# Performance work log

Measured on AMD Instinct MI355X. Metric: run time of the kernel, lower is better.

Reference implementation:

```python
import jax, jax.numpy as jnp
import numpy as np

B, S, E, H = 4, 2048, 1024, 16
D = E // H  # head dim = 64


def setup_inputs() -> dict:
    key = jax.random.key(0)
    ks = jax.random.split(key, 8)
    scale = 0.02
    return {
        "query": jax.random.normal(ks[0], (B, S, E), jnp.float32),
        "keys": jax.random.normal(ks[1], (B, S, E), jnp.float32),
        "values": jax.random.normal(ks[2], (B, S, E), jnp.float32),
        "mask": jnp.ones((B, 1, 1, S), jnp.int32),
        "Wq": jax.random.normal(ks[3], (D, D), jnp.float32) * scale,
        "Wk": jax.random.normal(ks[4], (D, D), jnp.float32) * scale,
        "Wv": jax.random.normal(ks[5], (D, D), jnp.float32) * scale,
        "Wf": jax.random.normal(ks[6], (E, E), jnp.float32) * scale,
        "bf": jax.random.normal(ks[7], (E,), jnp.float32) * scale,
    }


def reference(query, keys, values, mask, Wq, Wk, Wv, Wf, bf):
    b, sq, _ = query.shape
    sk = keys.shape[1]
    # reshape to heads: [b, s, H, D]
    q = query.reshape(b, sq, H, D)
    k = keys.reshape(b, sk, H, D)
    v = values.reshape(b, sk, H, D)
    # per-head linear projections (torch Linear: x @ W.T, no bias)
    q = jnp.einsum('bshd,ed->bshe', q, Wq)
    k = jnp.einsum('bshd,ed->bshe', k, Wk)
    v = jnp.einsum('bshd,ed->bshe', v, Wv)
    # scores [b, h, q, k]
    scores = jnp.einsum('bqhd,bkhd->bhqk', q, k)
    scores = jnp.where(mask == 0, -jnp.inf, scores)
    attn = jax.nn.softmax(scores / jnp.sqrt(jnp.float32(D)), axis=3)
    # context [b, q, h, d] -> [b, q, E]
    ctx = jnp.einsum('bhqk,bkhd->bqhd', attn, v).reshape(b, sq, E)
    return ctx @ Wf.T + bf
```

## Files before the change

kernel.cpp:

```cpp
#include <hip/hip_runtime.h>

#define B_ 4
#define S_ 2048
#define E_ 1024
#define H_ 16
#define D_ 64

typedef unsigned short u16;
typedef unsigned int u32;
typedef __bf16 bf16x8 __attribute__((ext_vector_type(8)));
typedef float f32x4 __attribute__((ext_vector_type(4)));
typedef u16 u16x8 __attribute__((ext_vector_type(8)));
typedef u16 u16x4 __attribute__((ext_vector_type(4)));

#if defined(__has_builtin)
#if __has_builtin(__builtin_amdgcn_exp2f)
#define EXP2F(x) __builtin_amdgcn_exp2f(x)
#else
#define EXP2F(x) exp2f(x)
#endif
#else
#define EXP2F(x) exp2f(x)
#endif

__device__ __forceinline__ u16 bfbits(float f) {
  __bf16 h = (__bf16)f;
  return __builtin_bit_cast(u16, h);
}
__device__ __forceinline__ f32x4 mfma16(bf16x8 a, bf16x8 b, f32x4 c) {
  return __builtin_amdgcn_mfma_f32_16x16x32_bf16(a, b, c, 0, 0, 0);
}
__device__ __forceinline__ bf16x8 lds_ld8(const u16* base, int off) {
  return *reinterpret_cast<const bf16x8*>(reinterpret_cast<const char*>(base) + off);
}
__device__ __forceinline__ void gload_lds16(const u16* g, u16* l) {
  __builtin_amdgcn_global_load_lds((const __attribute__((address_space(1))) void*)g,
                                   (__attribute__((address_space(3))) void*)l, 16, 0, 0);
}

__global__ __launch_bounds__(256) void proj_kernel(
    const float* __restrict__ qin, const float* __restrict__ kin, const float* __restrict__ vin,
    const float* __restrict__ Wq, const float* __restrict__ Wk, const float* __restrict__ Wv,
    const float* __restrict__ Wf,
    u16* __restrict__ qo, u16* __restrict__ ko, u16* __restrict__ vo, u16* __restrict__ wfo)
{
  const int t = threadIdx.x;
  const int tensor = blockIdx.z >> 2, b = blockIdx.z & 3;

  if (tensor == 3) {
    int chunk = ((blockIdx.z & 3) * 16 + blockIdx.y) * 16 + blockIdx.x;
    int i = chunk * 256 + t;
    float4 f = reinterpret_cast<const float4*>(Wf)[i];
    u16x4 h4;
    h4[0] = bfbits(f.x); h4[1] = bfbits(f.y); h4[2] = bfbits(f.z); h4[3] = bfbits(f.w);
    reinterpret_cast<u16x4*>(wfo)[i] = h4;
    return;
  }

  __shared__ __align__(16) u16 Al[128 * 64];
  __shared__ __align__(16) u16 Wl[64 * 64];
  const int w = t >> 6, l = t & 63, lg = l >> 4, ln = l & 15;
  const int h = blockIdx.y, s0 = blockIdx.x * 128;

  const float* x; const float* W; float scale;
  if (tensor == 0)      { x = qin; W = Wq; scale = 0.125f * 1.44269504f; }
  else if (tensor == 1) { x = kin; W = Wk; scale = 1.0f; }
  else                  { x = vin; W = Wv; scale = 1.0f; }

  {
    const int e = t >> 2, d0 = (t & 3) * 16;
    const float4* wr = reinterpret_cast<const float4*>(W + e * 64 + d0);
    float4 f0 = wr[0], f1 = wr[1], f2 = wr[2], f3 = wr[3];
    u16x8 p0, p1;
    p0[0]=bfbits(f0.x*scale); p0[1]=bfbits(f0.y*scale); p0[2]=bfbits(f0.z*scale); p0[3]=bfbits(f0.w*scale);
    p0[4]=bfbits(f1.x*scale); p0[5]=bfbits(f1.y*scale); p0[6]=bfbits(f1.z*scale); p0[7]=bfbits(f1.w*scale);
    p1[0]=bfbits(f2.x*scale); p1[1]=bfbits(f2.y*scale); p1[2]=bfbits(f2.z*scale); p1[3]=bfbits(f2.w*scale);
    p1[4]=bfbits(f3.x*scale); p1[5]=bfbits(f3.y*scale); p1[6]=bfbits(f3.z*scale); p1[7]=bfbits(f3.w*scale);
    *reinterpret_cast<u16x8*>(reinterpret_cast<char*>(Wl) + ((e*128 + d0*2     ) ^ ((e & 7) << 4))) = p0;
    *reinterpret_cast<u16x8*>(reinterpret_cast<char*>(Wl) + ((e*128 + d0*2 + 16) ^ ((e & 7) << 4))) = p1;
  }
  {
    const int row = t >> 1, d0 = (t & 1) * 32;
    const float4* xr = reinterpret_cast<const float4*>(x + ((size_t)(b * S_ + s0 + row)) * E_ + h * D_ + d0);
    #pragma unroll
    for (int c = 0; c < 4; ++c) {
      float4 f0 = xr[2 * c], f1 = xr[2 * c + 1];
      u16x8 pk;
      pk[0]=bfbits(f0.x); pk[1]=bfbits(f0.y); pk[2]=bfbits(f0.z); pk[3]=bfbits(f0.w);
      pk[4]=bfbits(f1.x); pk[5]=bfbits(f1.y); pk[6]=bfbits(f1.z); pk[7]=bfbits(f1.w);
      *reinterpret_cast<u16x8*>(reinterpret_cast<char*>(Al) +
          ((row * 128 + (d0 + 8 * c) * 2) ^ ((row & 7) << 4))) = pk;
    }
  }
  __syncthreads();

  bf16x8 wb[4][2];
  #pragma unroll
  for (int nn = 0; nn < 4; ++nn) {
    int brow = nn * 16 + ln;
    int bo = (brow * 128 + lg * 16) ^ ((ln & 7) << 4);
    wb[nn][0] = lds_ld8(Wl, bo);
    wb[nn][1] = lds_ld8(Wl, bo ^ 64);
  }
  f32x4 acc[2][4] = {};
  #pragma unroll
  for (int sub = 0; sub < 2; ++sub) {
    int arow = 32 * w + 16 * sub + ln;
    int ao = (arow * 128 + lg * 16) ^ ((ln & 7) << 4);
    bf16x8 a0 = lds_ld8(Al, ao), a1 = lds_ld8(Al, ao ^ 64);
    #pragma unroll
    for (int nn = 0; nn < 4; ++nn) {
      acc[sub][nn] = mfma16(a0, wb[nn][0], acc[sub][nn]);
      acc[sub][nn] = mfma16(a1, wb[nn][1], acc[sub][nn]);
    }
  }

  if (tensor < 2) {
    u16* o = (tensor == 0) ? qo : ko;
    const size_t hb = ((size_t)(b * H_ + h)) * (S_ * D_);
    #pragma unroll
    for (int sub = 0; sub < 2; ++sub)
      #pragma unroll
      for (int nn = 0; nn < 4; ++nn)
        #pragma unroll
        for (int r = 0; r < 4; ++r)
          o[hb + (size_t)(s0 + 32*w + 16*sub + 4*lg + r) * D_ + nn*16 + ln] = bfbits(acc[sub][nn][r]);
  } else {
    const size_t hb = ((size_t)(b * H_ + h)) * (D_ * S_);
    #pragma unroll
    for (int sub = 0; sub < 2; ++sub)
      #pragma unroll
      for (int nn = 0; nn < 4; ++nn)
        #pragma unroll
        for (int r = 0; r < 4; ++r) {
          int scol = s0 + 32*w + 16*sub + 4*lg + r;
          int sl = scol & 63;
          int c = (sl & 3) | (((sl >> 4) & 1) << 2) | (((sl >> 2) & 3) << 3) | ((sl >> 5) << 5);
          vo[hb + (size_t)(nn*16 + ln) * S_ + (scol & ~63) + c] = bfbits(acc[sub][nn][r]);
        }
  }
}

#define COMPUTE_TILE(KT, BUF)                                                  \
  {                                                                            \
    const u16* Kc = &Kl[BUF][0];                                               \
    const u16* Vc = &Vl[BUF][0];                                               \
    f32x4 sc[2][4];                                                            \
    __builtin_amdgcn_s_setprio(1);                                             \
    _Pragma("unroll")                                                          \
    for (int kn = 0; kn < 4; ++kn) {                                           \
      int o0 = ((ln * 128 + lg * 16) ^ ((ln & 7) << 4)) + kn * 2048;           \
      bf16x8 ka0 = lds_ld8(Kc, o0), ka1 = lds_ld8(Kc, o0 ^ 64);                \
      _Pragma("unroll")                                                        \
      for (int sub = 0; sub < 2; ++sub) {                                      \
        f32x4 z = {0.f, 0.f, 0.f, 0.f};                                        \
        z = mfma16(ka0, qb[sub][0], z);                                        \
        z = mfma16(ka1, qb[sub][1], z);                                        \
        sc[sub][kn] = z;                                                       \
      }                                                                        \
    }                                                                          \
    __builtin_amdgcn_s_setprio(0);                                             \
    if (!allone) {                                                             \
      const int kv0 = (KT) * 64;                                               \
      _Pragma("unroll")                                                        \
      for (int kn = 0; kn < 4; ++kn) {                                         \
        const int4 m4 = *reinterpret_cast<const int4*>(                        \
            mask + b * S_ + kv0 + kn * 16 + lg * 4);                           \
        const int* mp = reinterpret_cast<const int*>(&m4);                     \
        _Pragma("unroll")                                                      \
        for (int r = 0; r < 4; ++r)                                            \
          if (mp[r] == 0) { sc[0][kn][r] = -1e30f; sc[1][kn][r] = -1e30f; }    \
      }                                                                        \
    }                                                                          \
    bf16x8 pa[2][2];                                                           \
    _Pragma("unroll")                                                          \
    for (int sub = 0; sub < 2; ++sub)                                          \
      _Pragma("unroll")                                                        \
      for (int kn = 0; kn < 4; ++kn)                                           \
        _Pragma("unroll")                                                      \
        for (int r = 0; r < 4; ++r)                                            \
          pa[sub][kn >> 1][(kn & 1) * 4 + r] = (__bf16)EXP2F(sc[sub][kn][r]);  \
    __builtin_amdgcn_s_setprio(1);                                             \
    _Pragma("unroll")                                                          \
    for (int sub = 0; sub < 2; ++sub) {                                        \
      lacc[sub] = mfma16(pa[sub][0], ones, lacc[sub]);                         \
      lacc[sub] = mfma16(pa[sub][1], ones, lacc[sub]);                         \
    }                                                                          \
    _Pragma("unroll")                                                          \
    for (int kh = 0; kh < 2; ++kh)                                             \
      _Pragma("unroll")                                                        \
      for (int dn = 0; dn < 4; ++dn) {                                         \
        int vo0 = ((ln * 128 + 16 * lg + 64 * kh) ^ ((ln & 7) << 4)) + dn * 2048; \
        bf16x8 vb = lds_ld8(Vc, vo0);                                          \
        _Pragma("unroll")                                                      \
        for (int sub = 0; sub < 2; ++sub)                                      \
          oacc[sub][dn] = mfma16(pa[sub][kh], vb, oacc[sub][dn]);              \
      }                                                                        \
    __builtin_amdgcn_s_setprio(0);                                             \
  }

__global__ __launch_bounds__(512, 4) void attn_kernel(
    const u16* __restrict__ qw,
    const u16* __restrict__ kw,
    const u16* __restrict__ vtw,
    const int* __restrict__ mask,
    u16* __restrict__ ctx)
{
  __shared__ __align__(16) u16 Kl[4][64 * 64];
  __shared__ __align__(16) u16 Vl[4][64 * 64];
  __shared__ int s_allone;

  const int t = threadIdx.x, w = t >> 6, l = t & 63, lg = l >> 4, ln = l & 15;
  const int hb = blockIdx.x;
  const int b = hb >> 4;
  const int q0 = blockIdx.y * 256;
  const size_t koff = (size_t)hb * (S_ * D_);
  const size_t voff = (size_t)hb * (D_ * S_);

  if (t == 0) s_allone = 1;
  __syncthreads();

  const int srow = t >> 3, scol = (t & 7) ^ ((t >> 3) & 7);
  const u16* kg = kw + koff + srow * D_ + scol * 8;
  const u16* vg = vtw + voff + (size_t)srow * S_ + scol * 8;
  u16* kd0 = &Kl[0][0] + t * 8;
  u16* vd0 = &Vl[0][0] + t * 8;

  gload_lds16(kg, kd0);
  gload_lds16(vg, vd0);
  gload_lds16(kg + 64 * D_, kd0 + 4096);
  gload_lds16(vg + 64,      vd0 + 4096);

  {
    const int4 m4 = *reinterpret_cast<const int4*>(mask + b * S_ + t * 4);
    if (!(m4.x && m4.y && m4.z && m4.w)) s_allone = 0;
  }

  bf16x8 qb[2][2];
  #pragma unroll
  for (int sub = 0; sub < 2; ++sub) {
    const u16* qp = qw + koff + (size_t)(q0 + 32*w + 16*sub + ln) * D_ + 8*lg;
    qb[sub][0] = *reinterpret_cast<const bf16x8*>(qp);
    qb[sub][1] = *reinterpret_cast<const bf16x8*>(qp + 32);
  }

  u16x8 ob;
  #pragma unroll
  for (int i = 0; i < 8; ++i) ob[i] = 0x3F80;
  const bf16x8 ones = __builtin_bit_cast(bf16x8, ob);

  f32x4 oacc[2][4] = {};
  f32x4 lacc[2] = {};

  asm volatile("s_waitcnt vmcnt(0)" ::: "memory");
  __syncthreads();
  const int allone = s_allone;

  for (int kt = 0; kt < 32; kt += 4) {
    if (kt + 2 < 32) {
      gload_lds16(kg + (kt + 2) * 64 * D_, kd0 + 2 * 4096);
      gload_lds16(vg + (kt + 2) * 64,      vd0 + 2 * 4096);
      gload_lds16(kg + (kt + 3) * 64 * D_, kd0 + 3 * 4096);
      gload_lds16(vg + (kt + 3) * 64,      vd0 + 3 * 4096);
    }
    COMPUTE_TILE(kt,     0)
    COMPUTE_TILE(kt + 1, 1)
    if (kt + 2 < 32) {
      asm volatile("s_waitcnt vmcnt(0)" ::: "memory");
      __syncthreads();
    }
    if (kt + 4 < 32) {
      gload_lds16(kg + (kt + 4) * 64 * D_, kd0);
      gload_lds16(vg + (kt + 4) * 64,      vd0);
      gload_lds16(kg + (kt + 5) * 64 * D_, kd0 + 4096);
      gload_lds16(vg + (kt + 5) * 64,      vd0 + 4096);
    }
    if (kt + 2 < 32) {
      COMPUTE_TILE(kt + 2, 2)
      COMPUTE_TILE(kt + 3, 3)
    }
    if (kt + 4 < 32) {
      asm volatile("s_waitcnt vmcnt(0)" ::: "memory");
      __syncthreads();
    }
  }

  #pragma unroll
  for (int sub = 0; sub < 2; ++sub) {
    #pragma unroll
    for (int r = 0; r < 4; ++r) {
      float linv = 1.f / lacc[sub][r];
      int qrow = q0 + 32 * w + 16 * sub + 4 * lg + r;
      size_t base = ((size_t)b * S_ + qrow) * E_ + (hb & 15) * D_;
      #pragma unroll
      for (int dn = 0; dn < 4; ++dn)
        ctx[base + dn * 16 + ln] = bfbits(oacc[sub][dn][r] * linv);
    }
  }
}

__global__ __launch_bounds__(256, 2) void outproj_kernel(
    const u16* __restrict__ ctx, const u16* __restrict__ wf,
    const float* __restrict__ bias, float* __restrict__ out)
{
  __shared__ __align__(16) u16 Al[2][128 * 64];
  __shared__ __align__(16) u16 Bl[2][128 * 64];
  const int t = threadIdx.x, w = t >> 6, l = t & 63, lg = l >> 4, ln = l & 15;
  const int wm = w >> 1, wn = w & 1;
  const int m0 = blockIdx.x * 128, n0 = blockIdx.y * 128;
  f32x4 acc[4][4] = {};

  const u16* ag[4]; const u16* bg[4]; int ldo[4];
  #pragma unroll
  for (int it = 0; it < 4; ++it) {
    int j = it * 256 + t, row = j >> 3, c = (j & 7) ^ (row & 7);
    ag[it] = ctx + (size_t)(m0 + row) * E_ + c * 8;
    bg[it] = wf  + (size_t)(n0 + row) * E_ + c * 8;
    ldo[it] = j * 8;
  }
  #pragma unroll
  for (int it = 0; it < 4; ++it) {
    gload_lds16(ag[it], &Al[0][0] + ldo[it]);
    gload_lds16(bg[it], &Bl[0][0] + ldo[it]);
  }
  asm volatile("s_waitcnt vmcnt(0)" ::: "memory");
  __syncthreads();

  int cur = 0;
  for (int kt = 0; kt < E_ / 64; ++kt) {
    if (kt + 1 < E_ / 64) {
      const int k0 = (kt + 1) * 64;
      #pragma unroll
      for (int it = 0; it < 4; ++it) {
        gload_lds16(ag[it] + k0, &Al[cur ^ 1][0] + ldo[it]);
        gload_lds16(bg[it] + k0, &Bl[cur ^ 1][0] + ldo[it]);
      }
    }
    const u16* Ac = &Al[cur][0]; const u16* Bc = &Bl[cur][0];

    bf16x8 af[4][2], bff[4][2];
    #pragma unroll
    for (int ms = 0; ms < 4; ++ms) {
      int ar = 64 * wm + 16 * ms + ln;
      int ao = (ar * 128 + lg * 16) ^ ((ln & 7) << 4);
      af[ms][0] = lds_ld8(Ac, ao); af[ms][1] = lds_ld8(Ac, ao ^ 64);
    }
    #pragma unroll
    for (int ns = 0; ns < 4; ++ns) {
      int br = 64 * wn + 16 * ns + ln;
      int bo = (br * 128 + lg * 16) ^ ((ln & 7) << 4);
      bff[ns][0] = lds_ld8(Bc, bo); bff[ns][1] = lds_ld8(Bc, bo ^ 64);
    }
    __builtin_amdgcn_s_setprio(1);
    #pragma unroll
    for (int ms = 0; ms < 4; ++ms)
      #pragma unroll
      for (int ns = 0; ns < 4; ++ns) {
        acc[ms][ns] = mfma16(af[ms][0], bff[ns][0], acc[ms][ns]);
        acc[ms][ns] = mfma16(af[ms][1], bff[ns][1], acc[ms][ns]);
      }
    __builtin_amdgcn_s_setprio(0);

    if (kt + 1 < E_ / 64) {
      asm volatile("s_waitcnt vmcnt(0)" ::: "memory");
      __syncthreads();
      cur ^= 1;
    }
  }

  #pragma unroll
  for (int ns = 0; ns < 4; ++ns) {
    float bv = bias[n0 + 64 * wn + 16 * ns + ln];
    #pragma unroll
    for (int ms = 0; ms < 4; ++ms)
      #pragma unroll
      for (int r = 0; r < 4; ++r)
        out[(size_t)(m0 + 64*wm + 16*ms + 4*lg + r) * E_ + n0 + 64*wn + 16*ns + ln] =
            acc[ms][ns][r] + bv;
  }
}

extern "C" void kernel_launch(void* const* d_in, const int* in_sizes, int n_in,
                              void* d_out, int out_size, void* d_ws, size_t ws_size,
                              hipStream_t stream)
{
  const float* q   = (const float*)d_in[0];
  const float* k   = (const float*)d_in[1];
  const float* v   = (const float*)d_in[2];
  const int*  mask = (const int*) d_in[3];
  const float* Wq  = (const float*)d_in[4];
  const float* Wk  = (const float*)d_in[5];
  const float* Wv  = (const float*)d_in[6];
  const float* Wf  = (const float*)d_in[7];
  const float* bfv = (const float*)d_in[8];
  float* out = (float*)d_out;

  const size_t NQKV = (size_t)B_ * H_ * S_ * D_;
  const size_t NCTX = (size_t)B_ * S_ * E_;
  u16* q_ws   = (u16*)d_ws;
  u16* k_ws   = q_ws + NQKV;
  u16* v_ws   = k_ws + NQKV;
  u16* ctx_ws = v_ws + NQKV;
  u16* wf_ws  = ctx_ws + NCTX;

  proj_kernel<<<dim3(S_ / 128, H_, 16), dim3(256), 0, stream>>>(
      q, k, v, Wq, Wk, Wv, Wf, q_ws, k_ws, v_ws, wf_ws);
  attn_kernel<<<dim3(B_ * H_, S_ / 256), dim3(512), 0, stream>>>(
      q_ws, k_ws, v_ws, mask, ctx_ws);
  outproj_kernel<<<dim3((B_ * S_) / 128, E_ / 128), dim3(256), 0, stream>>>(
      ctx_ws, wf_ws, bfv, out);
}
```

Before: 117.1 us.

## Load output-projection weights directly to registers and stage activations two tiles per barrier

The output projection GEMM no longer stages the weight tile through LDS. Each wave reads its Wf fragments straight from global memory into registers, relying on L2 reuse across blocks. The activation tile now uses four LDS buffers, so two k-tiles are loaded and consumed per barrier, halving the number of barriers and vmcnt waits. The cost is that global-load latency for the weights now sits inside the MFMA step, and the weight loads are less coalesced than the old LDS path.

```diff
diff --git a/kernel.cpp b/kernel.cpp
--- a/kernel.cpp
+++ b/kernel.cpp
@@ -299,74 +299,98 @@
   }
 }
 
+#define OSTEP(KT, BUF)                                                         \
+  {                                                                            \
+    const u16* Ac = &Al[BUF][0];                                               \
+    bf16x8 bfv[4][2];                                                          \
+    _Pragma("unroll")                                                          \
+    for (int ns = 0; ns < 4; ++ns) {                                           \
+      const u16* bp = wf + (size_t)(n0 + 64*wn + 16*ns + ln) * E_ + (KT)*64 + 8*lg; \
+      bfv[ns][0] = *reinterpret_cast<const bf16x8*>(bp);                       \
+      bfv[ns][1] = *reinterpret_cast<const bf16x8*>(bp + 32);                  \
+    }                                                                          \
+    bf16x8 af[4][2];                                                           \
+    _Pragma("unroll")                                                          \
+    for (int ms = 0; ms < 4; ++ms) {                                           \
+      int ar = 64 * wm + 16 * ms + ln;                                         \
+      int ao = (ar * 128 + lg * 16) ^ ((ln & 7) << 4);                         \
+      af[ms][0] = lds_ld8(Ac, ao);                                             \
+      af[ms][1] = lds_ld8(Ac, ao ^ 64);                                        \
+    }                                                                          \
+    __builtin_amdgcn_s_setprio(1);                                             \
+    _Pragma("unroll")                                                          \
+    for (int ms = 0; ms < 4; ++ms)                                             \
+      _Pragma("unroll")                                                        \
+      for (int ns = 0; ns < 4; ++ns) {                                         \
+        acc[ms][ns] = mfma16(af[ms][0], bfv[ns][0], acc[ms][ns]);              \
+        acc[ms][ns] = mfma16(af[ms][1], bfv[ns][1], acc[ms][ns]);              \
+      }                                                                        \
+    __builtin_amdgcn_s_setprio(0);                                             \
+  }
+
 __global__ __launch_bounds__(256, 2) void outproj_kernel(
     const u16* __restrict__ ctx, const u16* __restrict__ wf,
     const float* __restrict__ bias, float* __restrict__ out)
 {
-  __shared__ __align__(16) u16 Al[2][128 * 64];
-  __shared__ __align__(16) u16 Bl[2][128 * 64];
+  __shared__ __align__(16) u16 Al[4][128 * 64];
   const int t = threadIdx.x, w = t >> 6, l = t & 63, lg = l >> 4, ln = l & 15;
   const int wm = w >> 1, wn = w & 1;
   const int m0 = blockIdx.x * 128, n0 = blockIdx.y * 128;
   f32x4 acc[4][4] = {};
 
-  const u16* ag[4]; const u16* bg[4]; int ldo[4];
-  #pragma unroll
-  for (int it = 0; it < 4; ++it) {
-    int j = it * 256 + t, row = j >> 3, c = (j & 7) ^ (row & 7);
-    ag[it] = ctx + (size_t)(m0 + row) * E_ + c * 8;
-    bg[it] = wf  + (size_t)(n0 + row) * E_ + c * 8;
-    ldo[it] = j * 8;
-  }
-  #pragma unroll
-  for (int it = 0; it < 4; ++it) {
-    gload_lds16(ag[it], &Al[0][0] + ldo[it]);
-    gload_lds16(bg[it], &Bl[0][0] + ldo[it]);
-  }
+  const u16* ag0; const u16* ag1; const u16* ag2; const u16* ag3;
+  int ldo0, ldo1, ldo2, ldo3;
+  {
+    int j0 = t,        r0 = j0 >> 3, c0 = (j0 & 7) ^ (r0 & 7);
+    int j1 = 256 + t,  r1 = j1 >> 3, c1 = (j1 & 7) ^ (r1 & 7);
+    int j2 = 512 + t,  r2 = j2 >> 3, c2 = (j2 & 7) ^ (r2 & 7);
+    int j3 = 768 + t,  r3 = j3 >> 3, c3 = (j3 & 7) ^ (r3 & 7);
+    ag0 = ctx + (size_t)(m0 + r0) * E_ + c0 * 8;  ldo0 = j0 * 8;
+    ag1 = ctx + (size_t)(m0 + r1) * E_ + c1 * 8;  ldo1 = j1 * 8;
+    ag2 = ctx + (size_t)(m0 + r2) * E_ + c2 * 8;  ldo2 = j2 * 8;
+    ag3 = ctx + (size_t)(m0 + r3) * E_ + c3 * 8;  ldo3 = j3 * 8;
+  }
+  u16* ad = &Al[0][0];
+
+#define STAGE_A(KT, BUF)                                                       \
+  {                                                                            \
+    const int k0_ = (KT) * 64;                                                 \
+    gload_lds16(ag0 + k0_, ad + (BUF) * 8192 + ldo0);                          \
+    gload_lds16(ag1 + k0_, ad + (BUF) * 8192 + ldo1);                          \
+    gload_lds16(ag2 + k0_, ad + (BUF) * 8192 + ldo2);                          \
+    gload_lds16(ag3 + k0_, ad + (BUF) * 8192 + ldo3);                          \
+  }
+
+  STAGE_A(0, 0)
+  STAGE_A(1, 1)
   asm volatile("s_waitcnt vmcnt(0)" ::: "memory");
   __syncthreads();
 
-  int cur = 0;
-  for (int kt = 0; kt < E_ / 64; ++kt) {
-    if (kt + 1 < E_ / 64) {
-      const int k0 = (kt + 1) * 64;
-      #pragma unroll
-      for (int it = 0; it < 4; ++it) {
-        gload_lds16(ag[it] + k0, &Al[cur ^ 1][0] + ldo[it]);
-        gload_lds16(bg[it] + k0, &Bl[cur ^ 1][0] + ldo[it]);
-      }
-    }
-    const u16* Ac = &Al[cur][0]; const u16* Bc = &Bl[cur][0];
-
-    bf16x8 af[4][2], bff[4][2];
-    #pragma unroll
-    for (int ms = 0; ms < 4; ++ms) {
-      int ar = 64 * wm + 16 * ms + ln;
-      int ao = (ar * 128 + lg * 16) ^ ((ln & 7) << 4);
-      af[ms][0] = lds_ld8(Ac, ao); af[ms][1] = lds_ld8(Ac, ao ^ 64);
-    }
-    #pragma unroll
-    for (int ns = 0; ns < 4; ++ns) {
-      int br = 64 * wn + 16 * ns + ln;
-      int bo = (br * 128 + lg * 16) ^ ((ln & 7) << 4);
-      bff[ns][0] = lds_ld8(Bc, bo); bff[ns][1] = lds_ld8(Bc, bo ^ 64);
-    }
-    __builtin_amdgcn_s_setprio(1);
-    #pragma unroll
-    for (int ms = 0; ms < 4; ++ms)
-      #pragma unroll
-      for (int ns = 0; ns < 4; ++ns) {
-        acc[ms][ns] = mfma16(af[ms][0], bff[ns][0], acc[ms][ns]);
-        acc[ms][ns] = mfma16(af[ms][1], bff[ns][1], acc[ms][ns]);
-      }
-    __builtin_amdgcn_s_setprio(0);
-
-    if (kt + 1 < E_ / 64) {
+  for (int kt = 0; kt < 16; kt += 4) {
+    if (kt + 2 < 16) {
+      STAGE_A(kt + 2, 2)
+      STAGE_A(kt + 3, 3)
+    }
+    OSTEP(kt,     0)
+    OSTEP(kt + 1, 1)
+    if (kt + 2 < 16) {
       asm volatile("s_waitcnt vmcnt(0)" ::: "memory");
       __syncthreads();
-      cur ^= 1;
-    }
-  }
+    }
+    if (kt + 4 < 16) {
+      STAGE_A(kt + 4, 0)
+      STAGE_A(kt + 5, 1)
+    }
+    if (kt + 2 < 16) {
+      OSTEP(kt + 2, 2)
+      OSTEP(kt + 3, 3)
+    }
+    if (kt + 4 < 16) {
+      asm volatile("s_waitcnt vmcnt(0)" ::: "memory");
+      __syncthreads();
+    }
+  }
+#undef STAGE_A
 
   #pragma unroll
   for (int ns = 0; ns < 4; ++ns) {
```

Result: slower. 132.9 us (+13.4%).
